# Kernel tuning notes

Hardware: AMD Instinct MI355X
Metric: run time of the kernel (lower is better)

Reference implementation:

```python
import jax, jax.numpy as jnp
import numpy as np

N, E, D = 40000, 640000, 128

def setup_inputs() -> dict:
    key = jax.random.key(0)
    ks = jax.random.split(key, 10)
    s = 0.02
    return {
        "node_hidden": jax.random.normal(ks[0], (N, D), jnp.float32),
        "edge_hidden": jax.random.normal(ks[1], (E, D), jnp.float32),
        "edge_index": jax.random.randint(ks[2], (2, E), 0, N, jnp.int32),
        "batch": jnp.zeros((N,), jnp.int32),
        "lin_w": jax.random.normal(ks[3], (D, D), jnp.float32) * s,
        "lin_b": jnp.zeros((D,), jnp.float32),
        "w1": jax.random.normal(ks[4], (D, 2 * D), jnp.float32) * s,
        "b1": jnp.zeros((2 * D,), jnp.float32),
        "w2": jax.random.normal(ks[5], (2 * D, D), jnp.float32) * s,
        "b2": jnp.zeros((D,), jnp.float32),
        "ln_g": jnp.ones((D,), jnp.float32),
        "ln_b": jnp.zeros((D,), jnp.float32),
    }

def _layernorm(x, g, b, eps=1e-5):
    mu = jnp.mean(x, axis=-1, keepdims=True)
    var = jnp.mean(jnp.square(x - mu), axis=-1, keepdims=True)
    return (x - mu) * jax.lax.rsqrt(var + eps) * g + b

def reference(node_hidden, edge_hidden, edge_index, batch,
              lin_w, lin_b, w1, b1, w2, b2, ln_g, ln_b):
    src, dst = edge_index[0], edge_index[1]
    # GINEConv: message = ReLU(x_src + Linear(edge_attr)), scatter-add at dst
    e = edge_hidden @ lin_w + lin_b                      # [E, D]
    msg = jax.nn.relu(node_hidden[src] + e)              # [E, D]
    aggr = jax.ops.segment_sum(msg, dst, num_segments=node_hidden.shape[0])
    h = node_hidden + aggr                               # (1+eps)*x + aggr, eps=0
    h = jax.nn.relu(h @ w1 + b1) @ w2 + b2               # GIN MLP
    h = _layernorm(h, ln_g, ln_b)
    # last_act=False; dropout is identity in eval mode
    return h + node_hidden
```

## Files before the change

kernel.cpp:

```cpp
#include <hip/hip_runtime.h>
#include <stdint.h>

#define NN 40000
#define EE 640000
#define DD 128

typedef __bf16 bf16x8 __attribute__((ext_vector_type(8)));
typedef float f32x4 __attribute__((ext_vector_type(4)));

__global__ __launch_bounds__(256) void init_prep(
        float4* __restrict__ aggr4, int4* __restrict__ counts4,
        const float* __restrict__ lw, const float* __restrict__ w1,
        const float* __restrict__ w2, char* __restrict__ wt,
        char* __restrict__ w1t, char* __restrict__ w2t) {
    const int b = blockIdx.x, t = threadIdx.x;
    const int tid = b * 256 + t;
    const float4 z4 = {0.f, 0.f, 0.f, 0.f};
    for (int i = tid; i < (NN * DD / 4); i += 327680)
        aggr4[i] = z4;
    if (tid < NN / 4) counts4[tid] = (int4){0, 0, 0, 0};

    if (b < 8) {
        const int j = tid >> 4, kc = tid & 15;
        bf16x8 p;
#pragma unroll
        for (int i = 0; i < 8; ++i) p[i] = (__bf16)lw[(kc * 8 + i) * 128 + j];
        *reinterpret_cast<bf16x8*>(wt + j * 256 + ((kc * 16) ^ ((j & 15) << 4))) = p;
    } else if (b < 24) {
        const int id = tid - 8 * 256;
        const int j = id >> 4, kc = id & 15;
        bf16x8 p;
#pragma unroll
        for (int i = 0; i < 8; ++i) p[i] = (__bf16)w1[(kc * 8 + i) * 256 + j];
        *reinterpret_cast<bf16x8*>(w1t + j * 256 + ((kc * 16) ^ ((j & 15) << 4))) = p;
    } else if (b < 40) {
        const int id = tid - 24 * 256;
        const int j = id >> 5, kc = id & 31;
        bf16x8 p;
#pragma unroll
        for (int i = 0; i < 8; ++i) p[i] = (__bf16)w2[(kc * 8 + i) * 128 + j];
        *reinterpret_cast<bf16x8*>(w2t + j * 512 + ((kc * 16) ^ ((j & 15) << 4))) = p;
    }
}

__global__ __launch_bounds__(256) void hist_kernel(const int* __restrict__ eidx,
                                                   int* __restrict__ counts,
                                                   int4* __restrict__ posl4) {
    const int i = blockIdx.x * 256 + threadIdx.x;
    const int4 d = reinterpret_cast<const int4*>(eidx + EE)[i];
    int4 p;
    p.x = atomicAdd(&counts[d.x], 1);
    p.y = atomicAdd(&counts[d.y], 1);
    p.z = atomicAdd(&counts[d.z], 1);
    p.w = atomicAdd(&counts[d.w], 1);
    posl4[i] = p;
}

__global__ __launch_bounds__(1024) void scanA(const int* __restrict__ counts,
                                              int* __restrict__ base,
                                              int* __restrict__ bsum) {
    __shared__ int part[1024];
    const int b = blockIdx.x, t = threadIdx.x;
    const int idx = b * 1024 + t;
    const int c = (idx < NN) ? counts[idx] : 0;
    part[t] = c;
    __syncthreads();
    for (int off = 1; off < 1024; off <<= 1) {
        const int v = (t >= off) ? part[t - off] : 0;
        __syncthreads();
        part[t] += v;
        __syncthreads();
    }
    if (idx < NN) base[idx] = part[t] - c;
    if (t == 1023) bsum[b] = part[1023];
}

__global__ __launch_bounds__(1024) void scanB(const int* __restrict__ bsum,
                                              int* __restrict__ base) {
    const int b = blockIdx.x, t = threadIdx.x;
    const int idx = b * 1024 + t;
    __shared__ int soff;
    if (t < 64) {
        int v = (t < b) ? bsum[t] : 0;
#pragma unroll
        for (int off = 1; off < 64; off <<= 1) v += __shfl_xor(v, off, 64);
        if (t == 0) soff = v;
    }
    __syncthreads();
    if (b > 0 && idx < NN) base[idx] += soff;
}

__global__ __launch_bounds__(256) void scatter_kernel(const int* __restrict__ eidx,
                                                      const int* __restrict__ base,
                                                      const int4* __restrict__ posl4,
                                                      uint2* __restrict__ meta) {
    const int i = blockIdx.x * 256 + threadIdx.x;
    const int4 s4 = reinterpret_cast<const int4*>(eidx)[i];
    const int4 d4 = reinterpret_cast<const int4*>(eidx + EE)[i];
    const int4 p4 = posl4[i];
    const unsigned e = 4u * i;
    const int b0 = base[d4.x], b1 = base[d4.y], b2 = base[d4.z], b3 = base[d4.w];
    meta[b0 + p4.x] = (uint2){e + 0, (unsigned)s4.x | ((unsigned)d4.x << 16)};
    meta[b1 + p4.y] = (uint2){e + 1, (unsigned)s4.y | ((unsigned)d4.y << 16)};
    meta[b2 + p4.z] = (uint2){e + 2, (unsigned)s4.z | ((unsigned)d4.z << 16)};
    meta[b3 + p4.w] = (uint2){e + 3, (unsigned)s4.w | ((unsigned)d4.w << 16)};
}

__global__ __launch_bounds__(512, 4) void edge_kernel(
        const float* __restrict__ node, const float* __restrict__ eh,
        const float* __restrict__ linb, const char* __restrict__ wt,
        const uint2* __restrict__ meta, float* __restrict__ aggr) {
    __shared__ __align__(16) char sMem[128 * 130 * 4];
    __shared__ int sDst[128];
    char* sA = sMem;
    char* sB = sMem + 128 * 256;
    float* accT = reinterpret_cast<float*>(sMem);
    const int t = threadIdx.x;
    const int e0 = blockIdx.x * 128;

    {
        const uint4* s = reinterpret_cast<const uint4*>(wt);
        uint4* d = reinterpret_cast<uint4*>(sB);
#pragma unroll
        for (int i = 0; i < 4; ++i) d[t + 512 * i] = s[t + 512 * i];
    }
    if (t < 128) sDst[t] = (int)(meta[e0 + t].y >> 16);

    {
        const int e = t >> 2, sub = t & 3;
        const int p = (int)meta[e0 + e].x;
        const float* row = eh + (size_t)p * DD;
        char* orow = sA + e * 256;
        const int sw = (e & 15) << 4;
#pragma unroll
        for (int i = 0; i < 4; ++i) {
            const int kc = sub + 4 * i;
            const float4 f0 = *reinterpret_cast<const float4*>(row + kc * 8);
            const float4 f1 = *reinterpret_cast<const float4*>(row + kc * 8 + 4);
            bf16x8 p8;
            p8[0] = (__bf16)f0.x; p8[1] = (__bf16)f0.y; p8[2] = (__bf16)f0.z; p8[3] = (__bf16)f0.w;
            p8[4] = (__bf16)f1.x; p8[5] = (__bf16)f1.y; p8[6] = (__bf16)f1.z; p8[7] = (__bf16)f1.w;
            *reinterpret_cast<bf16x8*>(orow + ((kc * 16) ^ sw)) = p8;
        }
    }

    const int col = t & 127, grp = t >> 7;
    float nv[32];
#pragma unroll
    for (int r = 0; r < 32; ++r) {
        const int src = (int)(meta[e0 + grp * 32 + r].y & 0xFFFFu);
        nv[r] = node[(size_t)src * DD + col];
    }

    __syncthreads();

    const int wave = t >> 6, l = t & 63;
    const int wm = wave >> 1, wn = wave & 1;
    const int lr = l & 15, lk = l >> 4;
    const int sw = lr << 4;
    f32x4 acc[2][4];
#pragma unroll
    for (int m = 0; m < 2; ++m)
#pragma unroll
        for (int n = 0; n < 4; ++n) acc[m][n] = (f32x4){0.f, 0.f, 0.f, 0.f};

#pragma unroll
    for (int ks = 0; ks < 4; ++ks) {
        const int kb = ks * 64 + lk * 16;
        bf16x8 a[2], b[4];
#pragma unroll
        for (int m = 0; m < 2; ++m) {
            const int e = wm * 32 + m * 16 + lr;
            a[m] = *reinterpret_cast<const bf16x8*>(sA + e * 256 + (kb ^ sw));
        }
#pragma unroll
        for (int n = 0; n < 4; ++n) {
            const int j = wn * 64 + n * 16 + lr;
            b[n] = *reinterpret_cast<const bf16x8*>(sB + j * 256 + (kb ^ sw));
        }
#pragma unroll
        for (int m = 0; m < 2; ++m)
#pragma unroll
            for (int n = 0; n < 4; ++n)
                acc[m][n] = __builtin_amdgcn_mfma_f32_16x16x32_bf16(a[m], b[n], acc[m][n], 0, 0, 0);
    }
    __syncthreads();

#pragma unroll
    for (int m = 0; m < 2; ++m)
#pragma unroll
        for (int n = 0; n < 4; ++n)
#pragma unroll
            for (int q = 0; q < 4; ++q) {
                const int row = wm * 32 + m * 16 + lk * 4 + q;
                const int cc = wn * 64 + n * 16 + lr;
                accT[row * 130 + cc] = acc[m][n][q];
            }
    __syncthreads();

    {
        const float lbv = linb[col];
        float run = 0.f;
        int cur = sDst[grp * 32];
#pragma unroll
        for (int r = 0; r < 32; ++r) {
            const int row = grp * 32 + r;
            const float v = fmaxf(accT[row * 130 + col] + lbv + nv[r], 0.f);
            const int d = sDst[row];
            if (d != cur) {
                atomicAdd(&aggr[(size_t)cur * DD + col], run);
                run = 0.f;
                cur = d;
            }
            run += v;
        }
        atomicAdd(&aggr[(size_t)cur * DD + col], run);
    }
}

__global__ __launch_bounds__(256) void mlp_kernel(
        const float* __restrict__ node, const float* __restrict__ aggr,
        const char* __restrict__ w1t, const char* __restrict__ w2t,
        const float* __restrict__ b1, const float* __restrict__ b2,
        const float* __restrict__ lng, const float* __restrict__ lnb,
        float* __restrict__ out) {
    __shared__ __align__(16) char sMem[64 * 132 * 4];
    char* sHhi = sMem;
    char* sHlo = sMem + 64 * 256;
    char* sT1  = sMem;
    float* accT = reinterpret_cast<float*>(sMem);
    const int t = threadIdx.x;
    const int n0 = blockIdx.x * 64;

    {
        const int e = t >> 2, sub = t & 3;
        const float* np = node + (size_t)(n0 + e) * DD;
        const float* ap = aggr + (size_t)(n0 + e) * DD;
        char* ohi = sHhi + e * 256;
        char* olo = sHlo + e * 256;
        const int sw = (e & 15) << 4;
#pragma unroll
        for (int i = 0; i < 4; ++i) {
            const int kc = sub + 4 * i;
            const float4 a0 = *reinterpret_cast<const float4*>(np + kc * 8);
            const float4 a1 = *reinterpret_cast<const float4*>(np + kc * 8 + 4);
            const float4 g0 = *reinterpret_cast<const float4*>(ap + kc * 8);
            const float4 g1 = *reinterpret_cast<const float4*>(ap + kc * 8 + 4);
            float s8[8] = {a0.x + g0.x, a0.y + g0.y, a0.z + g0.z, a0.w + g0.w,
                           a1.x + g1.x, a1.y + g1.y, a1.z + g1.z, a1.w + g1.w};
            bf16x8 ph, pl;
#pragma unroll
            for (int q = 0; q < 8; ++q) {
                const __bf16 hi = (__bf16)s8[q];
                ph[q] = hi;
                pl[q] = (__bf16)(s8[q] - (float)hi);
            }
            *reinterpret_cast<bf16x8*>(ohi + ((kc * 16) ^ sw)) = ph;
            *reinterpret_cast<bf16x8*>(olo + ((kc * 16) ^ sw)) = pl;
        }
    }
    __syncthreads();

    const int w = t >> 6, l = t & 63;
    const int lr = l & 15, lk = l >> 4;
    const int sw = lr << 4;
    const int jbase = w * 64;

    f32x4 acc1[4][4];
#pragma unroll
    for (int m = 0; m < 4; ++m)
#pragma unroll
        for (int n = 0; n < 4; ++n) acc1[m][n] = (f32x4){0.f, 0.f, 0.f, 0.f};
#pragma unroll
    for (int ks = 0; ks < 4; ++ks) {
        const int kb = ks * 64 + lk * 16;
        bf16x8 ahi[4], alo[4], b[4];
#pragma unroll
        for (int m = 0; m < 4; ++m) {
            ahi[m] = *reinterpret_cast<const bf16x8*>(sHhi + (m * 16 + lr) * 256 + (kb ^ sw));
            alo[m] = *reinterpret_cast<const bf16x8*>(sHlo + (m * 16 + lr) * 256 + (kb ^ sw));
        }
#pragma unroll
        for (int n = 0; n < 4; ++n) {
            const int j = jbase + n * 16 + lr;
            b[n] = *reinterpret_cast<const bf16x8*>(w1t + j * 256 + (kb ^ sw));
        }
#pragma unroll
        for (int m = 0; m < 4; ++m)
#pragma unroll
            for (int n = 0; n < 4; ++n) {
                acc1[m][n] = __builtin_amdgcn_mfma_f32_16x16x32_bf16(ahi[m], b[n], acc1[m][n], 0, 0, 0);
                acc1[m][n] = __builtin_amdgcn_mfma_f32_16x16x32_bf16(alo[m], b[n], acc1[m][n], 0, 0, 0);
            }
    }
    __syncthreads();

    {
        float bb[4];
#pragma unroll
        for (int n = 0; n < 4; ++n) bb[n] = b1[jbase + n * 16 + lr];
#pragma unroll
        for (int m = 0; m < 4; ++m)
#pragma unroll
            for (int n = 0; n < 4; ++n) {
                const int j = jbase + n * 16 + lr;
#pragma unroll
                for (int q = 0; q < 4; ++q) {
                    const int row = m * 16 + lk * 4 + q;
                    const float v = fmaxf(acc1[m][n][q] + bb[n], 0.f);
                    *reinterpret_cast<__bf16*>(sT1 + row * 512 +
                        ((((j >> 3) * 16) ^ ((row & 15) << 4)) + (j & 7) * 2)) = (__bf16)v;
                }
            }
    }
    __syncthreads();

    f32x4 acc2[4][2];
#pragma unroll
    for (int m = 0; m < 4; ++m)
#pragma unroll
        for (int n = 0; n < 2; ++n) acc2[m][n] = (f32x4){0.f, 0.f, 0.f, 0.f};
    {
        const int jb2 = w * 32;
#pragma unroll
        for (int ks = 0; ks < 8; ++ks) {
            const int kb = ks * 64 + lk * 16;
            bf16x8 a[4], b[2];
#pragma unroll
            for (int m = 0; m < 4; ++m)
                a[m] = *reinterpret_cast<const bf16x8*>(sT1 + (m * 16 + lr) * 512 + (kb ^ sw));
#pragma unroll
            for (int n = 0; n < 2; ++n) {
                const int j = jb2 + n * 16 + lr;
                b[n] = *reinterpret_cast<const bf16x8*>(w2t + j * 512 + (kb ^ sw));
            }
#pragma unroll
            for (int m = 0; m < 4; ++m)
#pragma unroll
                for (int n = 0; n < 2; ++n)
                    acc2[m][n] = __builtin_amdgcn_mfma_f32_16x16x32_bf16(a[m], b[n], acc2[m][n], 0, 0, 0);
        }
    }
    __syncthreads();

    {
        const int jb2 = w * 32;
        float bb[2];
#pragma unroll
        for (int n = 0; n < 2; ++n) bb[n] = b2[jb2 + n * 16 + lr];
#pragma unroll
        for (int m = 0; m < 4; ++m)
#pragma unroll
            for (int n = 0; n < 2; ++n)
#pragma unroll
                for (int q = 0; q < 4; ++q) {
                    const int row = m * 16 + lk * 4 + q;
                    accT[row * 132 + jb2 + n * 16 + lr] = acc2[m][n][q] + bb[n];
                }
    }
    __syncthreads();

    {
        const int nd = t >> 2, s = t & 3;
        float sum = 0.f, sq = 0.f;
#pragma unroll
        for (int i = 0; i < 32; ++i) {
            const float v = accT[nd * 132 + s * 32 + i];
            sum += v; sq += v * v;
        }
        sum += __shfl_xor(sum, 1, 64); sq += __shfl_xor(sq, 1, 64);
        sum += __shfl_xor(sum, 2, 64); sq += __shfl_xor(sq, 2, 64);
        const float mu  = sum * (1.f / 128.f);
        const float var = sq * (1.f / 128.f) - mu * mu;
        const float rs  = rsqrtf(var + 1e-5f);
        const float* nr = node + (size_t)(n0 + nd) * DD;
        float* orow = out + (size_t)(n0 + nd) * DD;
#pragma unroll
        for (int qq = 0; qq < 8; ++qq) {
            const int j = s * 32 + qq * 4;
            const float4 g  = *reinterpret_cast<const float4*>(&lng[j]);
            const float4 bbv = *reinterpret_cast<const float4*>(&lnb[j]);
            const float4 nvv = *reinterpret_cast<const float4*>(&nr[j]);
            float4 o;
            o.x = (accT[nd * 132 + j + 0] - mu) * rs * g.x + bbv.x + nvv.x;
            o.y = (accT[nd * 132 + j + 1] - mu) * rs * g.y + bbv.y + nvv.y;
            o.z = (accT[nd * 132 + j + 2] - mu) * rs * g.z + bbv.z + nvv.z;
            o.w = (accT[nd * 132 + j + 3] - mu) * rs * g.w + bbv.w + nvv.w;
            *reinterpret_cast<float4*>(&orow[j]) = o;
        }
    }
}

extern "C" void kernel_launch(void* const* d_in, const int* in_sizes, int n_in,
                              void* d_out, int out_size, void* d_ws, size_t ws_size,
                              hipStream_t stream) {
    const float* node  = (const float*)d_in[0];
    const float* eh    = (const float*)d_in[1];
    const int*   eidx  = (const int*)d_in[2];
    const float* lin_w = (const float*)d_in[4];
    const float* lin_b = (const float*)d_in[5];
    const float* w1    = (const float*)d_in[6];
    const float* b1    = (const float*)d_in[7];
    const float* w2    = (const float*)d_in[8];
    const float* b2    = (const float*)d_in[9];
    const float* ln_g  = (const float*)d_in[10];
    const float* ln_b  = (const float*)d_in[11];
    float* out = (float*)d_out;

    char* ws = (char*)d_ws;
    float* aggr    = (float*)ws;
    char*  wt      = ws + (size_t)NN * DD * 4;
    char*  w1t     = wt + 32768;
    char*  w2t     = w1t + 65536;
    int*   counts  = (int*)(w2t + 65536);
    int*   base    = counts + NN;
    int*   bsum    = base + NN;
    int*   posl    = bsum + 64;
    uint2* meta    = (uint2*)(posl + EE);

    init_prep<<<1280, 256, 0, stream>>>((float4*)aggr, (int4*)counts,
                                        lin_w, w1, w2, wt, w1t, w2t);
    hist_kernel<<<EE / 4 / 256, 256, 0, stream>>>(eidx, counts, (int4*)posl);
    scanA<<<40, 1024, 0, stream>>>(counts, base, bsum);
    scanB<<<40, 1024, 0, stream>>>(bsum, base);
    scatter_kernel<<<EE / 4 / 256, 256, 0, stream>>>(eidx, base, (const int4*)posl, meta);
    edge_kernel<<<EE / 128, 512, 0, stream>>>(node, eh, lin_b, wt, meta, aggr);
    mlp_kernel<<<NN / 64, 256, 0, stream>>>(node, aggr, w1t, w2t, b1, b2, ln_g, ln_b, out);
}
```

Before: 197.3 us.

## Replace global atomic histogram with per-block LDS packed-byte histograms and merge pass

Destination counting moves from global atomics into per-block LDS histograms, with four 8-bit counters packed into each uint. A new merge kernel takes a column-wise prefix over the 250 block histograms to produce per-block offsets and the total counts. The scatter kernel then adds the block offset to each edge's local byte rank. The intent is to remove contention on global atomics and shrink the rank buffer to bytes. In exchange it adds about 20MB of workspace traffic through a low-parallelism merge kernel, and it assumes no node has more than 255 incoming edges.

```diff
diff --git a/kernel.cpp b/kernel.cpp
--- a/kernel.cpp
+++ b/kernel.cpp
@@ -7,9 +7,11 @@
 
 typedef __bf16 bf16x8 __attribute__((ext_vector_type(8)));
 typedef float f32x4 __attribute__((ext_vector_type(4)));
+typedef unsigned int uint;
+typedef unsigned char uchar;
 
 __global__ __launch_bounds__(256) void init_prep(
-        float4* __restrict__ aggr4, int4* __restrict__ counts4,
+        float4* __restrict__ aggr4,
         const float* __restrict__ lw, const float* __restrict__ w1,
         const float* __restrict__ w2, char* __restrict__ wt,
         char* __restrict__ w1t, char* __restrict__ w2t) {
@@ -18,7 +20,6 @@
     const float4 z4 = {0.f, 0.f, 0.f, 0.f};
     for (int i = tid; i < (NN * DD / 4); i += 327680)
         aggr4[i] = z4;
-    if (tid < NN / 4) counts4[tid] = (int4){0, 0, 0, 0};
 
     if (b < 8) {
         const int j = tid >> 4, kc = tid & 15;
@@ -43,17 +44,48 @@
     }
 }
 
-__global__ __launch_bounds__(256) void hist_kernel(const int* __restrict__ eidx,
-                                                   int* __restrict__ counts,
-                                                   int4* __restrict__ posl4) {
-    const int i = blockIdx.x * 256 + threadIdx.x;
-    const int4 d = reinterpret_cast<const int4*>(eidx + EE)[i];
-    int4 p;
-    p.x = atomicAdd(&counts[d.x], 1);
-    p.y = atomicAdd(&counts[d.y], 1);
-    p.z = atomicAdd(&counts[d.z], 1);
-    p.w = atomicAdd(&counts[d.w], 1);
-    posl4[i] = p;
+__global__ __launch_bounds__(256) void hist_lds(const int* __restrict__ eidx,
+                                                uint* __restrict__ counts2d,
+                                                uchar* __restrict__ posl) {
+    __shared__ uint lh[10000];
+    const int t = threadIdx.x, blk = blockIdx.x;
+    for (int j = t; j < 10000; j += 256) lh[j] = 0u;
+    __syncthreads();
+    const int e0 = blk * 2560;
+    uchar rank[10];
+#pragma unroll
+    for (int i = 0; i < 10; ++i) {
+        const int d = eidx[EE + e0 + i * 256 + t];
+        const uint sh = (uint)(d & 3) * 8u;
+        const uint old = atomicAdd(&lh[d >> 2], 1u << sh);
+        rank[i] = (uchar)((old >> sh) & 0xFFu);
+    }
+#pragma unroll
+    for (int i = 0; i < 10; ++i) posl[e0 + i * 256 + t] = rank[i];
+    __syncthreads();
+    for (int j = t; j < 10000; j += 256)
+        counts2d[(size_t)blk * 10000 + j] = lh[j];
+}
+
+__global__ __launch_bounds__(256) void merge_kernel(const uint* __restrict__ counts2d,
+                                                    uint* __restrict__ base2d,
+                                                    int4* __restrict__ counts4) {
+    const int j = blockIdx.x * 256 + threadIdx.x;
+    if (j >= 10000) return;
+    uint pp = 0u;
+    for (int bc = 0; bc < 25; ++bc) {
+        uint v[10];
+#pragma unroll
+        for (int u = 0; u < 10; ++u)
+            v[u] = counts2d[(size_t)(bc * 10 + u) * 10000 + j];
+#pragma unroll
+        for (int u = 0; u < 10; ++u) {
+            base2d[(size_t)(bc * 10 + u) * 10000 + j] = pp;
+            pp += v[u];
+        }
+    }
+    counts4[j] = (int4){(int)(pp & 0xFFu), (int)((pp >> 8) & 0xFFu),
+                        (int)((pp >> 16) & 0xFFu), (int)((pp >> 24) & 0xFFu)};
 }
 
 __global__ __launch_bounds__(1024) void scanA(const int* __restrict__ counts,
@@ -92,18 +124,27 @@
 
 __global__ __launch_bounds__(256) void scatter_kernel(const int* __restrict__ eidx,
                                                       const int* __restrict__ base,
-                                                      const int4* __restrict__ posl4,
+                                                      const uint* __restrict__ base2d,
+                                                      const uchar* __restrict__ posl,
                                                       uint2* __restrict__ meta) {
     const int i = blockIdx.x * 256 + threadIdx.x;
     const int4 s4 = reinterpret_cast<const int4*>(eidx)[i];
     const int4 d4 = reinterpret_cast<const int4*>(eidx + EE)[i];
-    const int4 p4 = posl4[i];
+    const uchar4 p4 = reinterpret_cast<const uchar4*>(posl)[i];
     const unsigned e = 4u * i;
-    const int b0 = base[d4.x], b1 = base[d4.y], b2 = base[d4.z], b3 = base[d4.w];
-    meta[b0 + p4.x] = (uint2){e + 0, (unsigned)s4.x | ((unsigned)d4.x << 16)};
-    meta[b1 + p4.y] = (uint2){e + 1, (unsigned)s4.y | ((unsigned)d4.y << 16)};
-    meta[b2 + p4.z] = (uint2){e + 2, (unsigned)s4.z | ((unsigned)d4.z << 16)};
-    meta[b3 + p4.w] = (uint2){e + 3, (unsigned)s4.w | ((unsigned)d4.w << 16)};
+    const int blk = (int)(e / 2560u);
+    const size_t b2o = (size_t)blk * 10000;
+
+    const int ds[4] = {d4.x, d4.y, d4.z, d4.w};
+    const int ss[4] = {s4.x, s4.y, s4.z, s4.w};
+    const uchar rk[4] = {p4.x, p4.y, p4.z, p4.w};
+#pragma unroll
+    for (int k = 0; k < 4; ++k) {
+        const int d = ds[k];
+        const uint pref = (base2d[b2o + (d >> 2)] >> ((uint)(d & 3) * 8u)) & 0xFFu;
+        const int pos = base[d] + (int)pref + (int)rk[k];
+        meta[pos] = (uint2){e + (unsigned)k, (unsigned)ss[k] | ((unsigned)d << 16)};
+    }
 }
 
 __global__ __launch_bounds__(512, 4) void edge_kernel(
@@ -408,22 +449,24 @@
     float* out = (float*)d_out;
 
     char* ws = (char*)d_ws;
-    float* aggr    = (float*)ws;
-    char*  wt      = ws + (size_t)NN * DD * 4;
-    char*  w1t     = wt + 32768;
-    char*  w2t     = w1t + 65536;
-    int*   counts  = (int*)(w2t + 65536);
-    int*   base    = counts + NN;
-    int*   bsum    = base + NN;
-    int*   posl    = bsum + 64;
-    uint2* meta    = (uint2*)(posl + EE);
-
-    init_prep<<<1280, 256, 0, stream>>>((float4*)aggr, (int4*)counts,
-                                        lin_w, w1, w2, wt, w1t, w2t);
-    hist_kernel<<<EE / 4 / 256, 256, 0, stream>>>(eidx, counts, (int4*)posl);
+    float* aggr     = (float*)ws;
+    char*  wt       = ws + (size_t)NN * DD * 4;
+    char*  w1t      = wt + 32768;
+    char*  w2t      = w1t + 65536;
+    int*   counts   = (int*)(w2t + 65536);
+    int*   base     = counts + NN;
+    int*   bsum     = base + NN;
+    uchar* posl     = (uchar*)(bsum + 64);
+    uint*  counts2d = (uint*)(posl + EE);
+    uint*  base2d   = counts2d + 2500000;
+    uint2* meta     = (uint2*)(base2d + 2500000);
+
+    init_prep<<<1280, 256, 0, stream>>>((float4*)aggr, lin_w, w1, w2, wt, w1t, w2t);
+    hist_lds<<<250, 256, 0, stream>>>(eidx, counts2d, posl);
+    merge_kernel<<<40, 256, 0, stream>>>(counts2d, base2d, (int4*)counts);
     scanA<<<40, 1024, 0, stream>>>(counts, base, bsum);
     scanB<<<40, 1024, 0, stream>>>(bsum, base);
-    scatter_kernel<<<EE / 4 / 256, 256, 0, stream>>>(eidx, base, (const int4*)posl, meta);
+    scatter_kernel<<<EE / 4 / 256, 256, 0, stream>>>(eidx, base, base2d, posl, meta);
     edge_kernel<<<EE / 128, 512, 0, stream>>>(node, eh, lin_b, wt, meta, aggr);
     mlp_kernel<<<NN / 64, 256, 0, stream>>>(node, aggr, w1t, w2t, b1, b2, ln_g, ln_b, out);
 }
```

After: 193.0 us. 1.02x faster.
